# Kernel optimization log

Hardware: AMD Instinct MI355X
Metric: run time of the kernel (lower is better)

The kernel has to match this reference:

```python
import jax, jax.numpy as jnp
import numpy as np

C = 128                      # channels per irrep
LS = [0, 0, 1, 1, 2, 2]      # active irreps (0e,0o,1e,1o,2e,2o), sorted order
D = C * sum(2 * l + 1 for l in LS)  # 2304
N = 100000                   # nodes


def setup_inputs() -> dict:
    key = jax.random.key(0)
    ks = jax.random.split(key, 7)
    inp = {"x": jax.random.normal(ks[0], (N, D), dtype=jnp.float32)}
    scale = 1.0 / np.sqrt(C)
    for name, k in zip(["W0p", "W0m", "W1p", "W1m", "W2p", "W2m"], ks[1:]):
        inp[name] = jax.random.normal(k, (C, C), dtype=jnp.float32) * scale
    return inp


def reference(x, W0p, W0m, W1p, W1m, W2p, W2m):
    # Split flat features into per-(l,parity) blocks [N, C, 2l+1],
    # mix channels per irrep (movedim + Linear in torch == einsum here),
    # merge back and add residual.
    Ws = [W0p, W0m, W1p, W1m, W2p, W2m]
    idx = 0
    parts = []
    for l, W in zip(LS, Ws):
        d = C * (2 * l + 1)
        blk = x[:, idx:idx + d].reshape(-1, C, 2 * l + 1)  # [N, C, m]
        idx += d
        y = jnp.einsum('ncm,dc->ndm', blk, W)              # channel mix per m
        parts.append(y.reshape(-1, d))
    return x + jnp.concatenate(parts, axis=-1)
```

## Files before the change

kernel.cpp:

```cpp
#include <hip/hip_runtime.h>
#include <hip/hip_bf16.h>

typedef float f32x4 __attribute__((ext_vector_type(4)));
typedef short s16x8 __attribute__((ext_vector_type(8)));

__device__ __forceinline__ unsigned short f32_to_bf16(float f){
    union { float f; unsigned u; } v; v.f = f;
    unsigned r = v.u + 0x7fffu + ((v.u >> 16) & 1u);
    return (unsigned short)(r >> 16);
}
__device__ __forceinline__ unsigned pack2(float a, float b){
    float2 t; t.x = a; t.y = b;
    __hip_bfloat162 h = __float22bfloat162_rn(t);
    union { __hip_bfloat162 h; unsigned u; } c; c.h = h;
    return c.u;
}

template<int N> __device__ __forceinline__ void wait_vmcnt(){
    if constexpr (N == 0)       asm volatile("s_waitcnt vmcnt(0)"  ::: "memory");
    else if constexpr (N == 3)  asm volatile("s_waitcnt vmcnt(3)"  ::: "memory");
    else if constexpr (N == 4)  asm volatile("s_waitcnt vmcnt(4)"  ::: "memory");
    else if constexpr (N == 5)  asm volatile("s_waitcnt vmcnt(5)"  ::: "memory");
    else if constexpr (N == 6)  asm volatile("s_waitcnt vmcnt(6)"  ::: "memory");
    else if constexpr (N == 8)  asm volatile("s_waitcnt vmcnt(8)"  ::: "memory");
    else if constexpr (N == 10) asm volatile("s_waitcnt vmcnt(10)" ::: "memory");
    else static_assert(N == 0, "add wait case");
    __builtin_amdgcn_sched_barrier(0);
}

__device__ __forceinline__ void bar_sync(){
    asm volatile("s_waitcnt lgkmcnt(0)" ::: "memory");
    __builtin_amdgcn_s_barrier();
    __builtin_amdgcn_sched_barrier(0);
}

__device__ __forceinline__ void dma16(const float* g, float* l){
    __builtin_amdgcn_global_load_lds(
        (const __attribute__((address_space(1))) unsigned int*)g,
        (__attribute__((address_space(3))) unsigned int*)l, 16, 0, 0);
}

__global__ __launch_bounds__(256)
void wconv_kernel(const float* __restrict__ W0p, const float* __restrict__ W0m,
                  const float* __restrict__ W1p, const float* __restrict__ W1m,
                  const float* __restrict__ W2p, const float* __restrict__ W2m,
                  unsigned short* __restrict__ wbf)
{
    const int idx = blockIdx.x * 256 + threadIdx.x;
    const int w  = idx >> 14;
    const int rc = idx & 16383;
    const float* Wp;
    switch (w) {
        case 0: Wp = W0p; break;  case 1: Wp = W0m; break;
        case 2: Wp = W1p; break;  case 3: Wp = W1m; break;
        case 4: Wp = W2p; break;  default: Wp = W2m; break;
    }
    const float v = Wp[rc] + (((rc >> 7) == (rc & 127)) ? 1.0f : 0.0f);
    wbf[idx] = f32_to_bf16(v);
}

template<int ML, int NT, int WGS>
__global__ __launch_bounds__(256, 2)
void lx_dma(const float* __restrict__ x, const unsigned short* __restrict__ wbf,
            float* __restrict__ out, int yoff0, int yoff1, int w0, int ntiles)
{
    constexpr int BLK   = 128 * ML;
    constexpr int NTB   = NT * BLK;
    constexpr int DI    = NTB * 4 / 4096;
    constexpr int SI    = DI;
    constexpr int RROWS = NT * ML;
    constexpr int RTC   = (RROWS + 15) / 16;

    __shared__ __attribute__((aligned(16))) float lin[2][NTB];
    __shared__ __attribute__((aligned(16))) float lout[NTB];

    const int parity = blockIdx.y;
    const int yoff   = parity ? yoff1 : yoff0;
    const unsigned short* wb = wbf + (size_t)(w0 + parity) * 16384;

    const int tid = threadIdx.x;
    const int wv  = tid >> 6, ln = tid & 63;
    const int l16 = ln & 15,  lhi = ln >> 4;

    s16x8 bfr[4][2];
    #pragma unroll
    for (int s = 0; s < 4; ++s)
        #pragma unroll
        for (int tf = 0; tf < 2; ++tf)
            bfr[s][tf] = *reinterpret_cast<const s16x8*>(
                wb + (wv * 32 + tf * 16 + l16) * 128 + s * 32 + lhi * 8);

    int fbase[RTC];
    #pragma unroll
    for (int rt = 0; rt < RTC; ++rt) {
        const int row = rt * 16 + l16;
        const int nl  = row / ML;
        fbase[rt] = nl * BLK + (row - nl * ML);
    }

    auto dma_tile = [&](int t, int cur) {
        const float* gb = x + (size_t)t * NT * 2304 + yoff;
        float* lb = &lin[cur][0];
        #pragma unroll
        for (int j = 0; j < DI; ++j) {
            const int chunk = j * 4 + wv;
            const int dw = chunk * 256 + ln * 4;
            const int nl = dw / BLK;
            const int r  = dw - nl * BLK;
            dma16(gb + (size_t)nl * 2304 + r, lb + chunk * 256);
        }
    };
    auto flush_tile = [&](int t) {
        float* gb = out + (size_t)t * NT * 2304 + yoff;
        #pragma unroll
        for (int i = 0; i < SI; ++i) {
            const int dw = (i * 256 + tid) * 4;
            const int nl = dw / BLK;
            const int r  = dw - nl * BLK;
            *reinterpret_cast<float4*>(gb + (size_t)nl * 2304 + r) =
                *reinterpret_cast<const float4*>(&lout[dw]);
        }
    };

    const int tstart = blockIdx.x;
    int cur = 0, last = tstart;
    dma_tile(tstart, 0);
    if (tstart + WGS < ntiles) { dma_tile(tstart + WGS, 1); wait_vmcnt<DI>(); }
    else                       { wait_vmcnt<0>(); }
    bar_sync();

    bool first = true;
    for (int t = tstart; t < ntiles; t += WGS, cur ^= 1) {
        const bool has1 = (t + WGS)     < ntiles;
        const bool has2 = (t + 2 * WGS) < ntiles;

        f32x4 acc[RTC][2];
        #pragma unroll
        for (int rt = 0; rt < RTC; ++rt) {
            acc[rt][0] = (f32x4){0.f,0.f,0.f,0.f};
            acc[rt][1] = (f32x4){0.f,0.f,0.f,0.f};
        }
        const float* bp = &lin[cur][0];
        #pragma unroll
        for (int s = 0; s < 4; ++s) {
            const int ko = (s * 32 + lhi * 8) * ML;
            #pragma unroll
            for (int rt = 0; rt < RTC; ++rt) {
                float a[8];
                #pragma unroll
                for (int j = 0; j < 8; ++j) a[j] = bp[fbase[rt] + ko + j * ML];
                union { s16x8 v; unsigned u[4]; } af;
                af.u[0] = pack2(a[0], a[1]); af.u[1] = pack2(a[2], a[3]);
                af.u[2] = pack2(a[4], a[5]); af.u[3] = pack2(a[6], a[7]);
                acc[rt][0] = __builtin_amdgcn_mfma_f32_16x16x32_bf16(af.v, bfr[s][0], acc[rt][0], 0, 0, 0);
                acc[rt][1] = __builtin_amdgcn_mfma_f32_16x16x32_bf16(af.v, bfr[s][1], acc[rt][1], 0, 0, 0);
            }
        }

        if (!first) flush_tile(t - WGS);

        bar_sync();

        #pragma unroll
        for (int rt = 0; rt < RTC; ++rt)
            #pragma unroll
            for (int tf = 0; tf < 2; ++tf) {
                const int col = wv * 32 + tf * 16 + l16;
                #pragma unroll
                for (int j = 0; j < 4; ++j) {
                    const int row = rt * 16 + lhi * 4 + j;
                    if (row < RROWS) {
                        const int nl = row / ML;
                        lout[nl * BLK + col * ML + (row - nl * ML)] = acc[rt][tf][j];
                    }
                }
            }

        if (has2) dma_tile(t + 2 * WGS, cur);

        if (has1) {
            if (first) { if (has2) wait_vmcnt<DI>();      else wait_vmcnt<0>();  }
            else       { if (has2) wait_vmcnt<SI + DI>(); else wait_vmcnt<SI>(); }
        }
        bar_sync();
        first = false;
        last  = t;
    }
    flush_tile(last);
}

template<int WGS>
__global__ __launch_bounds__(256, 4)
void l0_dma(const float* __restrict__ x, const unsigned short* __restrict__ wbf,
            float* __restrict__ out, int ntiles)
{
    constexpr int NT = 16;
    constexpr int DI = 4;
    constexpr int SI = 4;

    __shared__ __attribute__((aligned(16))) float lin[2][NT * 256];

    const int tid = threadIdx.x;
    const int wv  = tid >> 6, ln = tid & 63;
    const int l16 = ln & 15,  lhi = ln >> 4;
    const int b     = wv >> 1;
    const int dbase = (wv & 1) * 64;
    const unsigned short* wb = wbf + b * 16384;

    s16x8 afr[4][4];
    #pragma unroll
    for (int s = 0; s < 4; ++s)
        #pragma unroll
        for (int dt = 0; dt < 4; ++dt)
            afr[s][dt] = *reinterpret_cast<const s16x8*>(
                wb + (dbase + dt * 16 + l16) * 128 + s * 32 + lhi * 8);

    auto dma_tile = [&](int t, int cur) {
        const float* gb = x + (size_t)t * NT * 2304;
        float* lb = &lin[cur][0];
        #pragma unroll
        for (int j = 0; j < DI; ++j) {
            const int chunk = j * 4 + wv;
            const int dw   = chunk * 256 + ln * 4;
            const int node = dw >> 8;
            const int r    = dw & 255;
            dma16(gb + (size_t)node * 2304 + (r ^ ((node & 7) << 2)), lb + chunk * 256);
        }
    };

    const int tstart = blockIdx.x;
    int cur = 0;
    dma_tile(tstart, 0);
    if (tstart + WGS < ntiles) { dma_tile(tstart + WGS, 1); wait_vmcnt<DI>(); }
    else                       { wait_vmcnt<0>(); }
    bar_sync();

    for (int t = tstart; t < ntiles; t += WGS, cur ^= 1) {
        const bool has1 = (t + WGS)     < ntiles;
        const bool has2 = (t + 2 * WGS) < ntiles;

        f32x4 acc[4];
        #pragma unroll
        for (int dt = 0; dt < 4; ++dt) acc[dt] = (f32x4){0.f,0.f,0.f,0.f};

        const float* bp = &lin[cur][0];
        const int nb = l16 * 256;
        const int sw = (l16 & 7) << 2;
        #pragma unroll
        for (int s = 0; s < 4; ++s) {
            const int c0 = b * 128 + s * 32 + lhi * 8;
            const float4 v0 = *reinterpret_cast<const float4*>(&bp[nb + ((c0    ) ^ sw)]);
            const float4 v1 = *reinterpret_cast<const float4*>(&bp[nb + ((c0 + 4) ^ sw)]);
            union { s16x8 v; unsigned u[4]; } bf;
            bf.u[0] = pack2(v0.x, v0.y); bf.u[1] = pack2(v0.z, v0.w);
            bf.u[2] = pack2(v1.x, v1.y); bf.u[3] = pack2(v1.z, v1.w);
            #pragma unroll
            for (int dt = 0; dt < 4; ++dt)
                acc[dt] = __builtin_amdgcn_mfma_f32_16x16x32_bf16(afr[s][dt], bf.v, acc[dt], 0, 0, 0);
        }

        bar_sync();

        float* dst = out + ((size_t)t * NT + l16) * 2304 + b * 128 + dbase + lhi * 4;
        #pragma unroll
        for (int dt = 0; dt < 4; ++dt) {
            float4 vv; vv.x = acc[dt][0]; vv.y = acc[dt][1];
                       vv.z = acc[dt][2]; vv.w = acc[dt][3];
            *reinterpret_cast<float4*>(dst + dt * 16) = vv;
        }

        if (has2) dma_tile(t + 2 * WGS, cur);
        if (has1) { if (has2) wait_vmcnt<SI + DI>(); else wait_vmcnt<SI>(); }
        bar_sync();
    }
}

extern "C" void kernel_launch(void* const* d_in, const int* in_sizes, int n_in,
                              void* d_out, int out_size, void* d_ws, size_t ws_size,
                              hipStream_t stream) {
    const float* x   = (const float*)d_in[0];
    const float* W0p = (const float*)d_in[1];
    const float* W0m = (const float*)d_in[2];
    const float* W1p = (const float*)d_in[3];
    const float* W1m = (const float*)d_in[4];
    const float* W2p = (const float*)d_in[5];
    const float* W2m = (const float*)d_in[6];
    float* out = (float*)d_out;
    unsigned short* wbf = (unsigned short*)d_ws;

    const int N = in_sizes[0] / 2304;

    wconv_kernel<<<384, 256, 0, stream>>>(W0p, W0m, W1p, W1m, W2p, W2m, wbf);

    lx_dma<5, 8, 256><<<dim3(256, 2), 256, 0, stream>>>(x, wbf, out, 1024, 1664, 4, N / 8);
    lx_dma<3, 8, 512><<<dim3(512, 2), 256, 0, stream>>>(x, wbf, out, 256,  640,  2, N / 8);
    l0_dma<1024>     <<<1024,         256, 0, stream>>>(x, wbf, out, N / 16);
}
```

Baseline: 434.0 us.

## Pre-pack input tiles to bf16 in LDS and single-buffer the lx DMA loop

In the l=1,2 kernels the fp32 input tile is no longer read with strided scalar LDS loads and packed per MFMA. Each tile is now read with float4 loads, transposed once, converted to bf16 into a padded LDS buffer, and the MFMA loop reads A fragments with single 16-byte loads. The input double buffer is replaced by a single buffer plus the bf16 staging buffer, allowing 3 workgroups per CU and a 384-block grid. The trade-off is extra barriers and less DMA/compute overlap: the store of each tile now finishes before the next prefetch is waited on.

```diff
diff --git a/kernel.cpp b/kernel.cpp
--- a/kernel.cpp
+++ b/kernel.cpp
@@ -21,9 +21,7 @@
     else if constexpr (N == 3)  asm volatile("s_waitcnt vmcnt(3)"  ::: "memory");
     else if constexpr (N == 4)  asm volatile("s_waitcnt vmcnt(4)"  ::: "memory");
     else if constexpr (N == 5)  asm volatile("s_waitcnt vmcnt(5)"  ::: "memory");
-    else if constexpr (N == 6)  asm volatile("s_waitcnt vmcnt(6)"  ::: "memory");
     else if constexpr (N == 8)  asm volatile("s_waitcnt vmcnt(8)"  ::: "memory");
-    else if constexpr (N == 10) asm volatile("s_waitcnt vmcnt(10)" ::: "memory");
     else static_assert(N == 0, "add wait case");
     __builtin_amdgcn_sched_barrier(0);
 }
@@ -59,8 +57,8 @@
     wbf[idx] = f32_to_bf16(v);
 }
 
-template<int ML, int NT, int WGS>
-__global__ __launch_bounds__(256, 2)
+template<int ML, int NT>
+__global__ __launch_bounds__(256, 3)
 void lx_dma(const float* __restrict__ x, const unsigned short* __restrict__ wbf,
             float* __restrict__ out, int yoff0, int yoff1, int w0, int ntiles)
 {
@@ -70,9 +68,14 @@
     constexpr int SI    = DI;
     constexpr int RROWS = NT * ML;
     constexpr int RTC   = (RROWS + 15) / 16;
-
-    __shared__ __attribute__((aligned(16))) float lin[2][NTB];
-    __shared__ __attribute__((aligned(16))) float lout[NTB];
+    constexpr int PR    = RTC * 16;
+    constexpr int LDSS  = 136;
+    constexpr int CPT   = NTB / 256;
+    constexpr int V4    = CPT / 4;
+
+    __shared__ __attribute__((aligned(16))) float          lin[NTB];
+    __shared__ __attribute__((aligned(16))) unsigned short lbf[PR * LDSS];
+    __shared__ __attribute__((aligned(16))) float          lout[NTB];
 
     const int parity = blockIdx.y;
     const int yoff   = parity ? yoff1 : yoff0;
@@ -90,24 +93,18 @@
             bfr[s][tf] = *reinterpret_cast<const s16x8*>(
                 wb + (wv * 32 + tf * 16 + l16) * 128 + s * 32 + lhi * 8);
 
-    int fbase[RTC];
-    #pragma unroll
-    for (int rt = 0; rt < RTC; ++rt) {
-        const int row = rt * 16 + l16;
-        const int nl  = row / ML;
-        fbase[rt] = nl * BLK + (row - nl * ML);
-    }
-
-    auto dma_tile = [&](int t, int cur) {
+    const int pnl = tid >> 5;
+    const int pc0 = (tid & 31) * 4;
+
+    auto dma_tile = [&](int t) {
         const float* gb = x + (size_t)t * NT * 2304 + yoff;
-        float* lb = &lin[cur][0];
         #pragma unroll
         for (int j = 0; j < DI; ++j) {
             const int chunk = j * 4 + wv;
             const int dw = chunk * 256 + ln * 4;
             const int nl = dw / BLK;
             const int r  = dw - nl * BLK;
-            dma16(gb + (size_t)nl * 2304 + r, lb + chunk * 256);
+            dma16(gb + (size_t)nl * 2304 + r, &lin[chunk * 256]);
         }
     };
     auto flush_tile = [&](int t) {
@@ -122,17 +119,31 @@
         }
     };
 
-    const int tstart = blockIdx.x;
-    int cur = 0, last = tstart;
-    dma_tile(tstart, 0);
-    if (tstart + WGS < ntiles) { dma_tile(tstart + WGS, 1); wait_vmcnt<DI>(); }
-    else                       { wait_vmcnt<0>(); }
+    int t = blockIdx.x;
+    dma_tile(t);
+    wait_vmcnt<0>();
     bar_sync();
 
-    bool first = true;
-    for (int t = tstart; t < ntiles; t += WGS, cur ^= 1) {
-        const bool has1 = (t + WGS)     < ntiles;
-        const bool has2 = (t + 2 * WGS) < ntiles;
+    while (true) {
+        {
+            float v[CPT];
+            const float* sp = &lin[pnl * BLK + pc0 * ML];
+            #pragma unroll
+            for (int i = 0; i < V4; ++i) {
+                const float4 t4 = *reinterpret_cast<const float4*>(sp + i * 4);
+                v[i*4+0] = t4.x; v[i*4+1] = t4.y; v[i*4+2] = t4.z; v[i*4+3] = t4.w;
+            }
+            #pragma unroll
+            for (int mm = 0; mm < ML; ++mm) {
+                unsigned* wp = reinterpret_cast<unsigned*>(&lbf[(pnl * ML + mm) * LDSS + pc0]);
+                wp[0] = pack2(v[mm],          v[ML + mm]);
+                wp[1] = pack2(v[2*ML + mm],   v[3*ML + mm]);
+            }
+        }
+        bar_sync();
+
+        const int nx = t + (int)gridDim.x;
+        if (nx < ntiles) dma_tile(nx);
 
         f32x4 acc[RTC][2];
         #pragma unroll
@@ -140,26 +151,17 @@
             acc[rt][0] = (f32x4){0.f,0.f,0.f,0.f};
             acc[rt][1] = (f32x4){0.f,0.f,0.f,0.f};
         }
-        const float* bp = &lin[cur][0];
         #pragma unroll
         for (int s = 0; s < 4; ++s) {
-            const int ko = (s * 32 + lhi * 8) * ML;
+            const int k0 = s * 32 + lhi * 8;
             #pragma unroll
             for (int rt = 0; rt < RTC; ++rt) {
-                float a[8];
-                #pragma unroll
-                for (int j = 0; j < 8; ++j) a[j] = bp[fbase[rt] + ko + j * ML];
-                union { s16x8 v; unsigned u[4]; } af;
-                af.u[0] = pack2(a[0], a[1]); af.u[1] = pack2(a[2], a[3]);
-                af.u[2] = pack2(a[4], a[5]); af.u[3] = pack2(a[6], a[7]);
-                acc[rt][0] = __builtin_amdgcn_mfma_f32_16x16x32_bf16(af.v, bfr[s][0], acc[rt][0], 0, 0, 0);
-                acc[rt][1] = __builtin_amdgcn_mfma_f32_16x16x32_bf16(af.v, bfr[s][1], acc[rt][1], 0, 0, 0);
-            }
-        }
-
-        if (!first) flush_tile(t - WGS);
-
-        bar_sync();
+                const s16x8 af = *reinterpret_cast<const s16x8*>(
+                    &lbf[(rt * 16 + l16) * LDSS + k0]);
+                acc[rt][0] = __builtin_amdgcn_mfma_f32_16x16x32_bf16(af, bfr[s][0], acc[rt][0], 0, 0, 0);
+                acc[rt][1] = __builtin_amdgcn_mfma_f32_16x16x32_bf16(af, bfr[s][1], acc[rt][1], 0, 0, 0);
+            }
+        }
 
         #pragma unroll
         for (int rt = 0; rt < RTC; ++rt)
@@ -175,18 +177,15 @@
                     }
                 }
             }
-
-        if (has2) dma_tile(t + 2 * WGS, cur);
-
-        if (has1) {
-            if (first) { if (has2) wait_vmcnt<DI>();      else wait_vmcnt<0>();  }
-            else       { if (has2) wait_vmcnt<SI + DI>(); else wait_vmcnt<SI>(); }
-        }
-        bar_sync();
-        first = false;
-        last  = t;
+        bar_sync();
+
+        flush_tile(t);
+
+        if (nx >= ntiles) break;
+        wait_vmcnt<SI>();
+        bar_sync();
+        t = nx;
     }
-    flush_tile(last);
 }
 
 template<int WGS>
@@ -292,7 +291,7 @@
 
     wconv_kernel<<<384, 256, 0, stream>>>(W0p, W0m, W1p, W1m, W2p, W2m, wbf);
 
-    lx_dma<5, 8, 256><<<dim3(256, 2), 256, 0, stream>>>(x, wbf, out, 1024, 1664, 4, N / 8);
-    lx_dma<3, 8, 512><<<dim3(512, 2), 256, 0, stream>>>(x, wbf, out, 256,  640,  2, N / 8);
-    l0_dma<1024>     <<<1024,         256, 0, stream>>>(x, wbf, out, N / 16);
-}
+    lx_dma<5, 8><<<dim3(384, 2), 256, 0, stream>>>(x, wbf, out, 1024, 1664, 4, N / 8);
+    lx_dma<3, 8><<<dim3(384, 2), 256, 0, stream>>>(x, wbf, out, 256,  640,  2, N / 8);
+    l0_dma<1024><<<1024,         256, 0, stream>>>(x, wbf, out, N / 16);
+}
```

Measured after the change: 399.6 us. 1.09x faster.
